# Optimization experiments

Hardware: AMD Instinct MI355X
Metric: run time of the kernel (lower is better)

The kernel has to match this reference:

```python
import jax, jax.numpy as jnp
import numpy as np

N_NODES = 50000
N_EDGES = 800000
STATE_DIM = 128
H1 = 96
H2 = 64


def setup_inputs() -> dict:
    key = jax.random.key(0)
    ks = jax.random.split(key, 10)
    x = jax.random.normal(ks[0], (N_NODES, STATE_DIM), dtype=jnp.float32)
    edge_index = jax.random.randint(ks[1], (2, N_EDGES), 0, N_NODES, dtype=jnp.int64)
    # GCNConv weight [in, out] and bias
    W1 = jax.random.normal(ks[2], (STATE_DIM, H1), dtype=jnp.float32) / np.sqrt(STATE_DIM)
    b1 = jnp.zeros((H1,), dtype=jnp.float32)
    lw1 = jax.random.normal(ks[3], (H1, H1), dtype=jnp.float32) / np.sqrt(H1)
    lb1 = jax.random.normal(ks[4], (H1,), dtype=jnp.float32) * 0.01
    lw2 = jax.random.normal(ks[5], (H1, H2), dtype=jnp.float32) / np.sqrt(H1)
    lb2 = jax.random.normal(ks[6], (H2,), dtype=jnp.float32) * 0.01
    lw3 = jax.random.normal(ks[7], (H2, 1), dtype=jnp.float32) / np.sqrt(H2)
    lb3 = jax.random.normal(ks[8], (1,), dtype=jnp.float32) * 0.01
    return {"x": x, "edge_index": edge_index, "W1": W1, "b1": b1,
            "lw1": lw1, "lb1": lb1, "lw2": lw2, "lb2": lb2, "lw3": lw3, "lb3": lb3}


def reference(x, edge_index, W1, b1, lw1, lb1, lw2, lb2, lw3, lb3):
    N = x.shape[0]
    loop = jnp.arange(N, dtype=edge_index.dtype)
    src = jnp.concatenate([edge_index[0], loop])
    dst = jnp.concatenate([edge_index[1], loop])
    deg = jax.ops.segment_sum(jnp.ones_like(dst, dtype=x.dtype), dst, num_segments=N)
    dinv = jnp.where(deg > 0, jax.lax.rsqrt(jnp.maximum(deg, 1.0)), 0.0)
    norm = dinv[src] * dinv[dst]  # [E+N]
    h = x @ W1  # [N, H1] transform before propagation
    agg = jax.ops.segment_sum(h[src] * norm[:, None], dst, num_segments=N) + b1
    out = jax.nn.relu(agg)            # [N, H1]
    g = jnp.sum(out, axis=0)          # sum pooling over nodes -> [H1]
    g = jax.nn.relu(g @ lw1 + lb1)
    g = jax.nn.relu(g @ lw2 + lb2)
    return g @ lw3 + lb3              # [1]
```

## Files before the change

### kernel.cpp

```cpp
#include <hip/hip_runtime.h>

#define N_NODES 50000
#define N_EDGES 800000
#define D_IN 128
#define H1 96
#define H2 64
#define GEMM_NODES 32
#define SCAN_BLK 256
#define N_SBLK ((N_NODES + SCAN_BLK - 1) / SCAN_BLK)

__global__ void count_deg_kernel(const int* __restrict__ dst, int* __restrict__ deg) {
    int i = blockIdx.x * blockDim.x + threadIdx.x;
    int stride = gridDim.x * blockDim.x;
    for (int e = i; e < N_EDGES; e += stride)
        atomicAdd(&deg[dst[e]], 1);
}

__global__ __launch_bounds__(SCAN_BLK) void deg_part_kernel(const int* __restrict__ deg,
                                                            int* __restrict__ block_sums) {
    __shared__ int s[SCAN_BLK];
    int t = threadIdx.x;
    int i = blockIdx.x * SCAN_BLK + t;
    s[t] = (i < N_NODES) ? deg[i] : 0;
    __syncthreads();
    for (int off = SCAN_BLK / 2; off > 0; off >>= 1) {
        if (t < off) s[t] += s[t + off];
        __syncthreads();
    }
    if (t == 0) block_sums[blockIdx.x] = s[0];
}

__global__ __launch_bounds__(SCAN_BLK) void block_scan_kernel(int* __restrict__ block_sums) {
    __shared__ int s[SCAN_BLK];
    int t = threadIdx.x;
    int v = (t < N_SBLK) ? block_sums[t] : 0;
    s[t] = v;
    __syncthreads();
    for (int off = 1; off < SCAN_BLK; off <<= 1) {
        int u = (t >= off) ? s[t - off] : 0;
        __syncthreads();
        s[t] += u;
        __syncthreads();
    }
    if (t < N_SBLK) block_sums[t] = s[t] - v;
}

__global__ __launch_bounds__(SCAN_BLK) void deg_scan_kernel(const int* __restrict__ deg,
                                                            const int* __restrict__ block_off,
                                                            int* __restrict__ row_start,
                                                            int* __restrict__ cursor,
                                                            float* __restrict__ dinv) {
    __shared__ int s[SCAN_BLK];
    int t = threadIdx.x;
    int i = blockIdx.x * SCAN_BLK + t;
    int v = (i < N_NODES) ? deg[i] : 0;
    s[t] = v;
    __syncthreads();
    for (int off = 1; off < SCAN_BLK; off <<= 1) {
        int u = (t >= off) ? s[t - off] : 0;
        __syncthreads();
        s[t] += u;
        __syncthreads();
    }
    int excl = s[t] - v + block_off[blockIdx.x];
    if (i < N_NODES) {
        row_start[i] = excl;
        cursor[i] = excl;
        dinv[i] = rsqrtf((float)v + 1.0f);
    }
    if (i == 0) row_start[N_NODES] = N_EDGES;
}

__global__ void scatter_kernel(const int* __restrict__ src, const int* __restrict__ dst,
                               int* __restrict__ cursor, int* __restrict__ sorted_src) {
    int i = blockIdx.x * blockDim.x + threadIdx.x;
    int stride = gridDim.x * blockDim.x;
    for (int e = i; e < N_EDGES; e += stride) {
        int d = dst[e];
        int pos = atomicAdd(&cursor[d], 1);
        sorted_src[pos] = src[e];
    }
}

__global__ __launch_bounds__(256) void gemm_kernel(const float* __restrict__ x,
                                                   const float* __restrict__ W1,
                                                   const float* __restrict__ dinv,
                                                   float* __restrict__ hs) {
    __shared__ float sW[D_IN * H1];
    __shared__ float sx[GEMM_NODES * D_IN];
    int tid = threadIdx.x;

    for (int i = tid; i < D_IN * H1 / 4; i += 256)
        ((float4*)sW)[i] = ((const float4*)W1)[i];

    int base = blockIdx.x * GEMM_NODES;
    const float4* x4 = (const float4*)x;
    for (int i = tid; i < GEMM_NODES * D_IN / 4; i += 256) {
        int n = base + i / (D_IN / 4);
        if (n < N_NODES) ((float4*)sx)[i] = x4[(size_t)base * (D_IN / 4) + i];
    }
    __syncthreads();

    int fg = tid & 31;
    int ng = tid >> 5;

    float acc[4][3];
#pragma unroll
    for (int i = 0; i < 4; ++i)
#pragma unroll
        for (int j = 0; j < 3; ++j) acc[i][j] = 0.0f;

#pragma unroll 4
    for (int k = 0; k < D_IN; ++k) {
        float w0 = sW[k * H1 + fg];
        float w1 = sW[k * H1 + fg + 32];
        float w2 = sW[k * H1 + fg + 64];
#pragma unroll
        for (int i = 0; i < 4; ++i) {
            float xv = sx[(ng * 4 + i) * D_IN + k];
            acc[i][0] = fmaf(xv, w0, acc[i][0]);
            acc[i][1] = fmaf(xv, w1, acc[i][1]);
            acc[i][2] = fmaf(xv, w2, acc[i][2]);
        }
    }

#pragma unroll
    for (int i = 0; i < 4; ++i) {
        int n = base + ng * 4 + i;
        if (n < N_NODES) {
            float dv = dinv[n];
            hs[(size_t)n * H1 + fg]      = acc[i][0] * dv;
            hs[(size_t)n * H1 + fg + 32] = acc[i][1] * dv;
            hs[(size_t)n * H1 + fg + 64] = acc[i][2] * dv;
        }
    }
}

__global__ __launch_bounds__(256) void agg_pool_kernel(const float* __restrict__ hs,
                                                       const int* __restrict__ row_start,
                                                       const int* __restrict__ sorted_src,
                                                       const float* __restrict__ dinv,
                                                       const float* __restrict__ b1,
                                                       float* __restrict__ g) {
    int tid = threadIdx.x;
    int grp = tid >> 7;
    int f = tid & 127;
    bool act = f < H1;
    float bf = act ? b1[f] : 0.0f;
    float gacc = 0.0f;

    for (int n = blockIdx.x * 2 + grp; n < N_NODES; n += gridDim.x * 2) {
        float acc = act ? hs[(size_t)n * H1 + f] : 0.0f;
        int e = row_start[n];
        int eend = row_start[n + 1];
        for (; e + 4 <= eend; e += 4) {
            int s0 = sorted_src[e];
            int s1 = sorted_src[e + 1];
            int s2 = sorted_src[e + 2];
            int s3 = sorted_src[e + 3];
            if (act) {
                float v0 = hs[(size_t)s0 * H1 + f];
                float v1 = hs[(size_t)s1 * H1 + f];
                float v2 = hs[(size_t)s2 * H1 + f];
                float v3 = hs[(size_t)s3 * H1 + f];
                acc += (v0 + v1) + (v2 + v3);
            }
        }
        for (; e < eend; ++e) {
            int s = sorted_src[e];
            if (act) acc += hs[(size_t)s * H1 + f];
        }
        if (act) gacc += fmaxf(fmaf(dinv[n], acc, bf), 0.0f);
    }

    __shared__ float sg[H1];
    if (grp == 0 && act) sg[f] = gacc;
    __syncthreads();
    if (grp == 1 && act) atomicAdd(&sg[f], gacc);
    __syncthreads();
    if (grp == 0 && act) atomicAdd(&g[f], sg[f]);
}

__global__ void mlp_kernel(const float* __restrict__ g,
                           const float* __restrict__ lw1, const float* __restrict__ lb1,
                           const float* __restrict__ lw2, const float* __restrict__ lb2,
                           const float* __restrict__ lw3, const float* __restrict__ lb3,
                           float* __restrict__ out) {
    __shared__ float sg[H1], v1[H1], v2[H2];
    int t = threadIdx.x;
    if (t < H1) sg[t] = g[t];
    __syncthreads();
    if (t < H1) {
        float a = lb1[t];
        for (int k = 0; k < H1; ++k) a = fmaf(sg[k], lw1[k * H1 + t], a);
        v1[t] = fmaxf(a, 0.0f);
    }
    __syncthreads();
    if (t < H2) {
        float a = lb2[t];
        for (int k = 0; k < H1; ++k) a = fmaf(v1[k], lw2[k * H2 + t], a);
        v2[t] = fmaxf(a, 0.0f);
    }
    __syncthreads();
    if (t == 0) {
        float a = lb3[0];
        for (int k = 0; k < H2; ++k) a = fmaf(v2[k], lw3[k], a);
        out[0] = a;
    }
}

extern "C" void kernel_launch(void* const* d_in, const int* in_sizes, int n_in,
                              void* d_out, int out_size, void* d_ws, size_t ws_size,
                              hipStream_t stream) {
    const float* x   = (const float*)d_in[0];
    const int*   ei  = (const int*)d_in[1];
    const float* W1  = (const float*)d_in[2];
    const float* b1  = (const float*)d_in[3];
    const float* lw1 = (const float*)d_in[4];
    const float* lb1 = (const float*)d_in[5];
    const float* lw2 = (const float*)d_in[6];
    const float* lb2 = (const float*)d_in[7];
    const float* lw3 = (const float*)d_in[8];
    const float* lb3 = (const float*)d_in[9];
    float* out = (float*)d_out;

    const int* src = ei;
    const int* dst = ei + N_EDGES;

    char* ws = (char*)d_ws;
    size_t off = 0;
    auto alloc = [&](size_t bytes) {
        char* p = ws + off;
        off = (off + bytes + 255) & ~(size_t)255;
        return p;
    };
    int*   deg        = (int*)alloc((size_t)N_NODES * sizeof(int));
    float* g          = (float*)alloc((size_t)H1 * sizeof(float));
    float* dinv       = (float*)alloc((size_t)N_NODES * sizeof(float));
    int*   row_start  = (int*)alloc((size_t)(N_NODES + 1) * sizeof(int));
    int*   cursor     = (int*)alloc((size_t)N_NODES * sizeof(int));
    int*   block_sums = (int*)alloc((size_t)N_SBLK * sizeof(int));
    int*   sorted_src = (int*)alloc((size_t)N_EDGES * sizeof(int));
    float* hs         = (float*)alloc((size_t)N_NODES * H1 * sizeof(float));
    (void)ws_size;

    hipMemsetAsync(deg, 0, (char*)(g + H1) - (char*)deg, stream);

    count_deg_kernel<<<2048, 256, 0, stream>>>(dst, deg);
    deg_part_kernel<<<N_SBLK, SCAN_BLK, 0, stream>>>(deg, block_sums);
    block_scan_kernel<<<1, SCAN_BLK, 0, stream>>>(block_sums);
    deg_scan_kernel<<<N_SBLK, SCAN_BLK, 0, stream>>>(deg, block_sums, row_start, cursor, dinv);
    scatter_kernel<<<2048, 256, 0, stream>>>(src, dst, cursor, sorted_src);

    gemm_kernel<<<(N_NODES + GEMM_NODES - 1) / GEMM_NODES, 256, 0, stream>>>(x, W1, dinv, hs);

    agg_pool_kernel<<<2048, 256, 0, stream>>>(hs, row_start, sorted_src, dinv, b1, g);

    mlp_kernel<<<1, 128, 0, stream>>>(g, lw1, lb1, lw2, lb2, lw3, lb3, out);
}
```

Before: 258.7 us.

## Store transformed node features in bf16 and gather packed pairs per wave

The GEMM output hs is now stored as bf16, which halves the gather traffic of the aggregation kernel. The aggregation is restructured so each 64-lane wave handles one node, with 48 active lanes each reading a packed uint32 holding two features and accumulating in fp32. The intent is to cut memory bandwidth and cache pressure in the random neighbour gather. The cost is reduced precision of the intermediate features and 16 idle lanes per wave.

```diff
diff --git a/kernel.cpp b/kernel.cpp
--- a/kernel.cpp
+++ b/kernel.cpp
@@ -1,13 +1,23 @@
 #include <hip/hip_runtime.h>
+#include <stdint.h>
 
 #define N_NODES 50000
 #define N_EDGES 800000
 #define D_IN 128
 #define H1 96
+#define H1P 48
 #define H2 64
 #define GEMM_NODES 32
 #define SCAN_BLK 256
 #define N_SBLK ((N_NODES + SCAN_BLK - 1) / SCAN_BLK)
+
+__device__ __forceinline__ uint16_t f2bf(float f) {
+    uint32_t u = __float_as_uint(f);
+    uint32_t r = (u + 0x7FFFu + ((u >> 16) & 1u)) >> 16;
+    return (uint16_t)r;
+}
+__device__ __forceinline__ float bf_lo(uint32_t v) { return __uint_as_float(v << 16); }
+__device__ __forceinline__ float bf_hi(uint32_t v) { return __uint_as_float(v & 0xFFFF0000u); }
 
 __global__ void count_deg_kernel(const int* __restrict__ dst, int* __restrict__ deg) {
     int i = blockIdx.x * blockDim.x + threadIdx.x;
@@ -85,7 +95,7 @@
 __global__ __launch_bounds__(256) void gemm_kernel(const float* __restrict__ x,
                                                    const float* __restrict__ W1,
                                                    const float* __restrict__ dinv,
-                                                   float* __restrict__ hs) {
+                                                   uint16_t* __restrict__ hs) {
     __shared__ float sW[D_IN * H1];
     __shared__ float sx[GEMM_NODES * D_IN];
     int tid = threadIdx.x;
@@ -129,56 +139,77 @@
         int n = base + ng * 4 + i;
         if (n < N_NODES) {
             float dv = dinv[n];
-            hs[(size_t)n * H1 + fg]      = acc[i][0] * dv;
-            hs[(size_t)n * H1 + fg + 32] = acc[i][1] * dv;
-            hs[(size_t)n * H1 + fg + 64] = acc[i][2] * dv;
-        }
-    }
-}
-
-__global__ __launch_bounds__(256) void agg_pool_kernel(const float* __restrict__ hs,
+            hs[(size_t)n * H1 + fg]      = f2bf(acc[i][0] * dv);
+            hs[(size_t)n * H1 + fg + 32] = f2bf(acc[i][1] * dv);
+            hs[(size_t)n * H1 + fg + 64] = f2bf(acc[i][2] * dv);
+        }
+    }
+}
+
+__global__ __launch_bounds__(256) void agg_pool_kernel(const uint32_t* __restrict__ hs2,
                                                        const int* __restrict__ row_start,
                                                        const int* __restrict__ sorted_src,
                                                        const float* __restrict__ dinv,
                                                        const float* __restrict__ b1,
                                                        float* __restrict__ g) {
     int tid = threadIdx.x;
-    int grp = tid >> 7;
-    int f = tid & 127;
-    bool act = f < H1;
-    float bf = act ? b1[f] : 0.0f;
-    float gacc = 0.0f;
-
-    for (int n = blockIdx.x * 2 + grp; n < N_NODES; n += gridDim.x * 2) {
-        float acc = act ? hs[(size_t)n * H1 + f] : 0.0f;
+    int wave = tid >> 6;
+    int j = tid & 63;
+    bool act = j < H1P;
+    float b0 = 0.0f, b1v = 0.0f;
+    if (act) { b0 = b1[2 * j]; b1v = b1[2 * j + 1]; }
+    float g0 = 0.0f, g1 = 0.0f;
+
+    int wid = blockIdx.x * 4 + wave;
+    int nw = gridDim.x * 4;
+    for (int n = wid; n < N_NODES; n += nw) {
+        float a0 = 0.0f, a1 = 0.0f;
+        if (act) {
+            uint32_t v = hs2[n * H1P + j];
+            a0 = bf_lo(v); a1 = bf_hi(v);
+        }
         int e = row_start[n];
-        int eend = row_start[n + 1];
-        for (; e + 4 <= eend; e += 4) {
+        int ee = row_start[n + 1];
+        for (; e + 4 <= ee; e += 4) {
             int s0 = sorted_src[e];
             int s1 = sorted_src[e + 1];
             int s2 = sorted_src[e + 2];
             int s3 = sorted_src[e + 3];
             if (act) {
-                float v0 = hs[(size_t)s0 * H1 + f];
-                float v1 = hs[(size_t)s1 * H1 + f];
-                float v2 = hs[(size_t)s2 * H1 + f];
-                float v3 = hs[(size_t)s3 * H1 + f];
-                acc += (v0 + v1) + (v2 + v3);
+                uint32_t v0 = hs2[s0 * H1P + j];
+                uint32_t v1 = hs2[s1 * H1P + j];
+                uint32_t v2 = hs2[s2 * H1P + j];
+                uint32_t v3 = hs2[s3 * H1P + j];
+                a0 += (bf_lo(v0) + bf_lo(v1)) + (bf_lo(v2) + bf_lo(v3));
+                a1 += (bf_hi(v0) + bf_hi(v1)) + (bf_hi(v2) + bf_hi(v3));
             }
         }
-        for (; e < eend; ++e) {
+        for (; e < ee; ++e) {
             int s = sorted_src[e];
-            if (act) acc += hs[(size_t)s * H1 + f];
-        }
-        if (act) gacc += fmaxf(fmaf(dinv[n], acc, bf), 0.0f);
+            if (act) {
+                uint32_t v = hs2[s * H1P + j];
+                a0 += bf_lo(v); a1 += bf_hi(v);
+            }
+        }
+        float dv = dinv[n];
+        if (act) {
+            g0 += fmaxf(fmaf(dv, a0, b0), 0.0f);
+            g1 += fmaxf(fmaf(dv, a1, b1v), 0.0f);
+        }
     }
 
     __shared__ float sg[H1];
-    if (grp == 0 && act) sg[f] = gacc;
-    __syncthreads();
-    if (grp == 1 && act) atomicAdd(&sg[f], gacc);
-    __syncthreads();
-    if (grp == 0 && act) atomicAdd(&g[f], sg[f]);
+    if (wave == 0 && act) { sg[2 * j] = g0; sg[2 * j + 1] = g1; }
+    __syncthreads();
+    if (wave != 0 && act) {
+        atomicAdd(&sg[2 * j], g0);
+        atomicAdd(&sg[2 * j + 1], g1);
+    }
+    __syncthreads();
+    if (wave == 0 && act) {
+        atomicAdd(&g[2 * j], sg[2 * j]);
+        atomicAdd(&g[2 * j + 1], sg[2 * j + 1]);
+    }
 }
 
 __global__ void mlp_kernel(const float* __restrict__ g,
@@ -234,14 +265,14 @@
         off = (off + bytes + 255) & ~(size_t)255;
         return p;
     };
-    int*   deg        = (int*)alloc((size_t)N_NODES * sizeof(int));
-    float* g          = (float*)alloc((size_t)H1 * sizeof(float));
-    float* dinv       = (float*)alloc((size_t)N_NODES * sizeof(float));
-    int*   row_start  = (int*)alloc((size_t)(N_NODES + 1) * sizeof(int));
-    int*   cursor     = (int*)alloc((size_t)N_NODES * sizeof(int));
-    int*   block_sums = (int*)alloc((size_t)N_SBLK * sizeof(int));
-    int*   sorted_src = (int*)alloc((size_t)N_EDGES * sizeof(int));
-    float* hs         = (float*)alloc((size_t)N_NODES * H1 * sizeof(float));
+    int*      deg        = (int*)alloc((size_t)N_NODES * sizeof(int));
+    float*    g          = (float*)alloc((size_t)H1 * sizeof(float));
+    float*    dinv       = (float*)alloc((size_t)N_NODES * sizeof(float));
+    int*      row_start  = (int*)alloc((size_t)(N_NODES + 1) * sizeof(int));
+    int*      cursor     = (int*)alloc((size_t)N_NODES * sizeof(int));
+    int*      block_sums = (int*)alloc((size_t)N_SBLK * sizeof(int));
+    int*      sorted_src = (int*)alloc((size_t)N_EDGES * sizeof(int));
+    uint16_t* hs         = (uint16_t*)alloc((size_t)N_NODES * H1 * sizeof(uint16_t));
     (void)ws_size;
 
     hipMemsetAsync(deg, 0, (char*)(g + H1) - (char*)deg, stream);
@@ -254,7 +285,7 @@
 
     gemm_kernel<<<(N_NODES + GEMM_NODES - 1) / GEMM_NODES, 256, 0, stream>>>(x, W1, dinv, hs);
 
-    agg_pool_kernel<<<2048, 256, 0, stream>>>(hs, row_start, sorted_src, dinv, b1, g);
+    agg_pool_kernel<<<2048, 256, 0, stream>>>((const uint32_t*)hs, row_start, sorted_src, dinv, b1, g);
 
     mlp_kernel<<<1, 128, 0, stream>>>(g, lw1, lb1, lw2, lb2, lw3, lb3, out);
 }
```

After: 278.2 us. 1.08x slower.

## Fuse GEMM with degree count and scatter with dinv scaling via block partitioning

Applied to the files above, without the earlier changes.

The GEMM is merged with degree counting into one launch that assigns block ranges by role. The dinv row scaling moves out of the GEMM into a second role-split kernel alongside the CSR scatter, so the GEMM no longer waits on the degree scan. The goal is fewer launches and concurrency between compute-bound and atomic-bound work. In exchange, h is re-read and re-written for scaling, an extra 19 MB of traffic. The MLP also stages its weights in shared memory.

```diff
diff --git a/kernel.cpp b/kernel.cpp
--- a/kernel.cpp
+++ b/kernel.cpp
@@ -1,4 +1,5 @@
 #include <hip/hip_runtime.h>
+#include <stdint.h>
 
 #define N_NODES 50000
 #define N_EDGES 800000
@@ -6,14 +7,79 @@
 #define H1 96
 #define H2 64
 #define GEMM_NODES 32
+#define GEMM_BLOCKS ((N_NODES + GEMM_NODES - 1) / GEMM_NODES)
+#define COUNT_BLOCKS 256
 #define SCAN_BLK 256
 #define N_SBLK ((N_NODES + SCAN_BLK - 1) / SCAN_BLK)
-
-__global__ void count_deg_kernel(const int* __restrict__ dst, int* __restrict__ deg) {
-    int i = blockIdx.x * blockDim.x + threadIdx.x;
-    int stride = gridDim.x * blockDim.x;
-    for (int e = i; e < N_EDGES; e += stride)
-        atomicAdd(&deg[dst[e]], 1);
+#define SCAT_BLOCKS 2048
+#define SCALE_BLOCKS 512
+
+__global__ __launch_bounds__(256) void k1_gemm_count(const float* __restrict__ x,
+                                                     const float* __restrict__ W1,
+                                                     float* __restrict__ h,
+                                                     const int* __restrict__ dst,
+                                                     int* __restrict__ deg) {
+    __shared__ float sW[D_IN * H1];
+    __shared__ float sx[GEMM_NODES * D_IN];
+    int tid = threadIdx.x;
+
+    if (blockIdx.x < GEMM_BLOCKS) {
+        for (int i = tid; i < D_IN * H1 / 4; i += 256)
+            ((float4*)sW)[i] = ((const float4*)W1)[i];
+
+        int base = blockIdx.x * GEMM_NODES;
+        const float4* x4 = (const float4*)x;
+        for (int i = tid; i < GEMM_NODES * D_IN / 4; i += 256) {
+            int n = base + i / (D_IN / 4);
+            if (n < N_NODES) ((float4*)sx)[i] = x4[(size_t)base * (D_IN / 4) + i];
+        }
+        __syncthreads();
+
+        int fg = tid & 31;
+        int ng = tid >> 5;
+
+        float acc[4][3];
+#pragma unroll
+        for (int i = 0; i < 4; ++i)
+#pragma unroll
+            for (int j = 0; j < 3; ++j) acc[i][j] = 0.0f;
+
+#pragma unroll 4
+        for (int k = 0; k < D_IN; ++k) {
+            float w0 = sW[k * H1 + fg];
+            float w1 = sW[k * H1 + fg + 32];
+            float w2 = sW[k * H1 + fg + 64];
+#pragma unroll
+            for (int i = 0; i < 4; ++i) {
+                float xv = sx[(ng * 4 + i) * D_IN + k];
+                acc[i][0] = fmaf(xv, w0, acc[i][0]);
+                acc[i][1] = fmaf(xv, w1, acc[i][1]);
+                acc[i][2] = fmaf(xv, w2, acc[i][2]);
+            }
+        }
+
+#pragma unroll
+        for (int i = 0; i < 4; ++i) {
+            int n = base + ng * 4 + i;
+            if (n < N_NODES) {
+                h[(size_t)n * H1 + fg]      = acc[i][0];
+                h[(size_t)n * H1 + fg + 32] = acc[i][1];
+                h[(size_t)n * H1 + fg + 64] = acc[i][2];
+            }
+        }
+    } else {
+        int bid = blockIdx.x - GEMM_BLOCKS;
+        int gid = bid * 256 + tid;
+        int stride = COUNT_BLOCKS * 256;
+        const int4* d4 = (const int4*)dst;
+        for (int i = gid; i < N_EDGES / 4; i += stride) {
+            int4 d = d4[i];
+            atomicAdd(&deg[d.x], 1);
+            atomicAdd(&deg[d.y], 1);
+            atomicAdd(&deg[d.z], 1);
+            atomicAdd(&deg[d.w], 1);
+        }
+    }
 }
 
 __global__ __launch_bounds__(SCAN_BLK) void deg_part_kernel(const int* __restrict__ deg,
@@ -71,67 +137,33 @@
     if (i == 0) row_start[N_NODES] = N_EDGES;
 }
 
-__global__ void scatter_kernel(const int* __restrict__ src, const int* __restrict__ dst,
-                               int* __restrict__ cursor, int* __restrict__ sorted_src) {
-    int i = blockIdx.x * blockDim.x + threadIdx.x;
-    int stride = gridDim.x * blockDim.x;
-    for (int e = i; e < N_EDGES; e += stride) {
-        int d = dst[e];
-        int pos = atomicAdd(&cursor[d], 1);
-        sorted_src[pos] = src[e];
-    }
-}
-
-__global__ __launch_bounds__(256) void gemm_kernel(const float* __restrict__ x,
-                                                   const float* __restrict__ W1,
-                                                   const float* __restrict__ dinv,
-                                                   float* __restrict__ hs) {
-    __shared__ float sW[D_IN * H1];
-    __shared__ float sx[GEMM_NODES * D_IN];
+__global__ __launch_bounds__(256) void k3_scatter_scale(const int* __restrict__ src,
+                                                        const int* __restrict__ dst,
+                                                        int* __restrict__ cursor,
+                                                        int* __restrict__ sorted_src,
+                                                        float* __restrict__ h,
+                                                        const float* __restrict__ dinv) {
     int tid = threadIdx.x;
-
-    for (int i = tid; i < D_IN * H1 / 4; i += 256)
-        ((float4*)sW)[i] = ((const float4*)W1)[i];
-
-    int base = blockIdx.x * GEMM_NODES;
-    const float4* x4 = (const float4*)x;
-    for (int i = tid; i < GEMM_NODES * D_IN / 4; i += 256) {
-        int n = base + i / (D_IN / 4);
-        if (n < N_NODES) ((float4*)sx)[i] = x4[(size_t)base * (D_IN / 4) + i];
-    }
-    __syncthreads();
-
-    int fg = tid & 31;
-    int ng = tid >> 5;
-
-    float acc[4][3];
-#pragma unroll
-    for (int i = 0; i < 4; ++i)
-#pragma unroll
-        for (int j = 0; j < 3; ++j) acc[i][j] = 0.0f;
-
-#pragma unroll 4
-    for (int k = 0; k < D_IN; ++k) {
-        float w0 = sW[k * H1 + fg];
-        float w1 = sW[k * H1 + fg + 32];
-        float w2 = sW[k * H1 + fg + 64];
-#pragma unroll
-        for (int i = 0; i < 4; ++i) {
-            float xv = sx[(ng * 4 + i) * D_IN + k];
-            acc[i][0] = fmaf(xv, w0, acc[i][0]);
-            acc[i][1] = fmaf(xv, w1, acc[i][1]);
-            acc[i][2] = fmaf(xv, w2, acc[i][2]);
-        }
-    }
-
-#pragma unroll
-    for (int i = 0; i < 4; ++i) {
-        int n = base + ng * 4 + i;
-        if (n < N_NODES) {
+    if (blockIdx.x < SCAT_BLOCKS) {
+        int gid = blockIdx.x * 256 + tid;
+        int stride = SCAT_BLOCKS * 256;
+        for (int e = gid; e < N_EDGES; e += stride) {
+            int d = dst[e];
+            int pos = atomicAdd(&cursor[d], 1);
+            sorted_src[pos] = src[e];
+        }
+    } else {
+        int bid = blockIdx.x - SCAT_BLOCKS;
+        int gid = bid * 256 + tid;
+        int stride = SCALE_BLOCKS * 256;
+        float4* h4 = (float4*)h;
+        const int TOT = N_NODES * (H1 / 4);
+        for (int i = gid; i < TOT; i += stride) {
+            int n = i / (H1 / 4);
             float dv = dinv[n];
-            hs[(size_t)n * H1 + fg]      = acc[i][0] * dv;
-            hs[(size_t)n * H1 + fg + 32] = acc[i][1] * dv;
-            hs[(size_t)n * H1 + fg + 64] = acc[i][2] * dv;
+            float4 v = h4[i];
+            v.x *= dv; v.y *= dv; v.z *= dv; v.w *= dv;
+            h4[i] = v;
         }
     }
 }
@@ -181,30 +213,41 @@
     if (grp == 0 && act) atomicAdd(&g[f], sg[f]);
 }
 
-__global__ void mlp_kernel(const float* __restrict__ g,
+__global__ __launch_bounds__(256) void mlp_kernel(const float* __restrict__ g,
                            const float* __restrict__ lw1, const float* __restrict__ lb1,
                            const float* __restrict__ lw2, const float* __restrict__ lb2,
                            const float* __restrict__ lw3, const float* __restrict__ lb3,
                            float* __restrict__ out) {
+    __shared__ float slw1[H1 * H1];
+    __shared__ float slw2[H1 * H2];
+    __shared__ float slw3[H2];
     __shared__ float sg[H1], v1[H1], v2[H2];
     int t = threadIdx.x;
+    for (int i = t; i < H1 * H1 / 4; i += 256)
+        ((float4*)slw1)[i] = ((const float4*)lw1)[i];
+    for (int i = t; i < H1 * H2 / 4; i += 256)
+        ((float4*)slw2)[i] = ((const float4*)lw2)[i];
+    if (t < H2) slw3[t] = lw3[t];
     if (t < H1) sg[t] = g[t];
     __syncthreads();
     if (t < H1) {
         float a = lb1[t];
-        for (int k = 0; k < H1; ++k) a = fmaf(sg[k], lw1[k * H1 + t], a);
+#pragma unroll 8
+        for (int k = 0; k < H1; ++k) a = fmaf(sg[k], slw1[k * H1 + t], a);
         v1[t] = fmaxf(a, 0.0f);
     }
     __syncthreads();
     if (t < H2) {
         float a = lb2[t];
-        for (int k = 0; k < H1; ++k) a = fmaf(v1[k], lw2[k * H2 + t], a);
+#pragma unroll 8
+        for (int k = 0; k < H1; ++k) a = fmaf(v1[k], slw2[k * H2 + t], a);
         v2[t] = fmaxf(a, 0.0f);
     }
     __syncthreads();
     if (t == 0) {
         float a = lb3[0];
-        for (int k = 0; k < H2; ++k) a = fmaf(v2[k], lw3[k], a);
+#pragma unroll 8
+        for (int k = 0; k < H2; ++k) a = fmaf(v2[k], slw3[k], a);
         out[0] = a;
     }
 }
@@ -241,20 +284,20 @@
     int*   cursor     = (int*)alloc((size_t)N_NODES * sizeof(int));
     int*   block_sums = (int*)alloc((size_t)N_SBLK * sizeof(int));
     int*   sorted_src = (int*)alloc((size_t)N_EDGES * sizeof(int));
-    float* hs         = (float*)alloc((size_t)N_NODES * H1 * sizeof(float));
+    float* h          = (float*)alloc((size_t)N_NODES * H1 * sizeof(float));
     (void)ws_size;
 
     hipMemsetAsync(deg, 0, (char*)(g + H1) - (char*)deg, stream);
 
-    count_deg_kernel<<<2048, 256, 0, stream>>>(dst, deg);
+    k1_gemm_count<<<GEMM_BLOCKS + COUNT_BLOCKS, 256, 0, stream>>>(x, W1, h, dst, deg);
+
     deg_part_kernel<<<N_SBLK, SCAN_BLK, 0, stream>>>(deg, block_sums);
     block_scan_kernel<<<1, SCAN_BLK, 0, stream>>>(block_sums);
     deg_scan_kernel<<<N_SBLK, SCAN_BLK, 0, stream>>>(deg, block_sums, row_start, cursor, dinv);
-    scatter_kernel<<<2048, 256, 0, stream>>>(src, dst, cursor, sorted_src);
-
-    gemm_kernel<<<(N_NODES + GEMM_NODES - 1) / GEMM_NODES, 256, 0, stream>>>(x, W1, dinv, hs);
-
-    agg_pool_kernel<<<2048, 256, 0, stream>>>(hs, row_start, sorted_src, dinv, b1, g);
-
-    mlp_kernel<<<1, 128, 0, stream>>>(g, lw1, lb1, lw2, lb2, lw3, lb3, out);
-}
+
+    k3_scatter_scale<<<SCAT_BLOCKS + SCALE_BLOCKS, 256, 0, stream>>>(src, dst, cursor, sorted_src, h, dinv);
+
+    agg_pool_kernel<<<2048, 256, 0, stream>>>(h, row_start, sorted_src, dinv, b1, g);
+
+    mlp_kernel<<<1, 256, 0, stream>>>(g, lw1, lb1, lw2, lb2, lw3, lb3, out);
+}
```

Result: faster. 248.3 us (-4.0%).

## Fuse scatter with GEMM, fold MLP into last aggregation block, vectorize degree count

Applied to the files above, without the earlier changes.

The edge scatter and the x@W1 GEMM now run as disjoint block ranges of one horizontally fused launch, so they can overlap. The GEMM reads W1 from global memory instead of staging it in LDS, which cuts LDS use per block and allows higher occupancy, at the cost of more global/L1 traffic. The MLP kernel is removed: the last block of the aggregation kernel, found through an atomic done counter, runs it. The degree count reads dst as int4 with fewer blocks.

```diff
diff --git a/kernel.cpp b/kernel.cpp
--- a/kernel.cpp
+++ b/kernel.cpp
@@ -1,4 +1,5 @@
 #include <hip/hip_runtime.h>
+#include <stdint.h>
 
 #define N_NODES 50000
 #define N_EDGES 800000
@@ -6,14 +7,24 @@
 #define H1 96
 #define H2 64
 #define GEMM_NODES 32
+#define GEMM_BLOCKS ((N_NODES + GEMM_NODES - 1) / GEMM_NODES)
+#define COUNT_BLOCKS 1024
 #define SCAN_BLK 256
 #define N_SBLK ((N_NODES + SCAN_BLK - 1) / SCAN_BLK)
+#define SCAT_BLOCKS 2048
+#define AGG_BLOCKS 2048
 
 __global__ void count_deg_kernel(const int* __restrict__ dst, int* __restrict__ deg) {
-    int i = blockIdx.x * blockDim.x + threadIdx.x;
-    int stride = gridDim.x * blockDim.x;
-    for (int e = i; e < N_EDGES; e += stride)
-        atomicAdd(&deg[dst[e]], 1);
+    int gid = blockIdx.x * 256 + threadIdx.x;
+    int stride = COUNT_BLOCKS * 256;
+    const int4* d4 = (const int4*)dst;
+    for (int i = gid; i < N_EDGES / 4; i += stride) {
+        int4 d = d4[i];
+        atomicAdd(&deg[d.x], 1);
+        atomicAdd(&deg[d.y], 1);
+        atomicAdd(&deg[d.z], 1);
+        atomicAdd(&deg[d.w], 1);
+    }
 }
 
 __global__ __launch_bounds__(SCAN_BLK) void deg_part_kernel(const int* __restrict__ deg,
@@ -71,67 +82,67 @@
     if (i == 0) row_start[N_NODES] = N_EDGES;
 }
 
-__global__ void scatter_kernel(const int* __restrict__ src, const int* __restrict__ dst,
-                               int* __restrict__ cursor, int* __restrict__ sorted_src) {
-    int i = blockIdx.x * blockDim.x + threadIdx.x;
-    int stride = gridDim.x * blockDim.x;
-    for (int e = i; e < N_EDGES; e += stride) {
-        int d = dst[e];
-        int pos = atomicAdd(&cursor[d], 1);
-        sorted_src[pos] = src[e];
-    }
-}
-
-__global__ __launch_bounds__(256) void gemm_kernel(const float* __restrict__ x,
-                                                   const float* __restrict__ W1,
-                                                   const float* __restrict__ dinv,
-                                                   float* __restrict__ hs) {
-    __shared__ float sW[D_IN * H1];
+__global__ __launch_bounds__(256) void k2_scatter_gemm(const int* __restrict__ src,
+                                                       const int* __restrict__ dst,
+                                                       int* __restrict__ cursor,
+                                                       int* __restrict__ sorted_src,
+                                                       const float* __restrict__ x,
+                                                       const float* __restrict__ W1,
+                                                       const float* __restrict__ dinv,
+                                                       float* __restrict__ hs) {
     __shared__ float sx[GEMM_NODES * D_IN];
     int tid = threadIdx.x;
 
-    for (int i = tid; i < D_IN * H1 / 4; i += 256)
-        ((float4*)sW)[i] = ((const float4*)W1)[i];
-
-    int base = blockIdx.x * GEMM_NODES;
-    const float4* x4 = (const float4*)x;
-    for (int i = tid; i < GEMM_NODES * D_IN / 4; i += 256) {
-        int n = base + i / (D_IN / 4);
-        if (n < N_NODES) ((float4*)sx)[i] = x4[(size_t)base * (D_IN / 4) + i];
-    }
-    __syncthreads();
-
-    int fg = tid & 31;
-    int ng = tid >> 5;
-
-    float acc[4][3];
-#pragma unroll
-    for (int i = 0; i < 4; ++i)
-#pragma unroll
-        for (int j = 0; j < 3; ++j) acc[i][j] = 0.0f;
+    if (blockIdx.x < SCAT_BLOCKS) {
+        int gid = blockIdx.x * 256 + tid;
+        int stride = SCAT_BLOCKS * 256;
+        for (int e = gid; e < N_EDGES; e += stride) {
+            int d = dst[e];
+            int pos = atomicAdd(&cursor[d], 1);
+            sorted_src[pos] = src[e];
+        }
+    } else {
+        int gblk = blockIdx.x - SCAT_BLOCKS;
+        int base = gblk * GEMM_NODES;
+        const float4* x4 = (const float4*)x;
+        for (int i = tid; i < GEMM_NODES * D_IN / 4; i += 256) {
+            int n = base + i / (D_IN / 4);
+            if (n < N_NODES) ((float4*)sx)[i] = x4[(size_t)base * (D_IN / 4) + i];
+        }
+        __syncthreads();
+
+        int fg = tid & 31;
+        int ng = tid >> 5;
+
+        float acc[4][3];
+#pragma unroll
+        for (int i = 0; i < 4; ++i)
+#pragma unroll
+            for (int j = 0; j < 3; ++j) acc[i][j] = 0.0f;
 
 #pragma unroll 4
-    for (int k = 0; k < D_IN; ++k) {
-        float w0 = sW[k * H1 + fg];
-        float w1 = sW[k * H1 + fg + 32];
-        float w2 = sW[k * H1 + fg + 64];
+        for (int k = 0; k < D_IN; ++k) {
+            float w0 = W1[k * H1 + fg];
+            float w1 = W1[k * H1 + fg + 32];
+            float w2 = W1[k * H1 + fg + 64];
+#pragma unroll
+            for (int i = 0; i < 4; ++i) {
+                float xv = sx[(ng * 4 + i) * D_IN + k];
+                acc[i][0] = fmaf(xv, w0, acc[i][0]);
+                acc[i][1] = fmaf(xv, w1, acc[i][1]);
+                acc[i][2] = fmaf(xv, w2, acc[i][2]);
+            }
+        }
+
 #pragma unroll
         for (int i = 0; i < 4; ++i) {
-            float xv = sx[(ng * 4 + i) * D_IN + k];
-            acc[i][0] = fmaf(xv, w0, acc[i][0]);
-            acc[i][1] = fmaf(xv, w1, acc[i][1]);
-            acc[i][2] = fmaf(xv, w2, acc[i][2]);
-        }
-    }
-
-#pragma unroll
-    for (int i = 0; i < 4; ++i) {
-        int n = base + ng * 4 + i;
-        if (n < N_NODES) {
-            float dv = dinv[n];
-            hs[(size_t)n * H1 + fg]      = acc[i][0] * dv;
-            hs[(size_t)n * H1 + fg + 32] = acc[i][1] * dv;
-            hs[(size_t)n * H1 + fg + 64] = acc[i][2] * dv;
+            int n = base + ng * 4 + i;
+            if (n < N_NODES) {
+                float dv = dinv[n];
+                hs[(size_t)n * H1 + fg]      = acc[i][0] * dv;
+                hs[(size_t)n * H1 + fg + 32] = acc[i][1] * dv;
+                hs[(size_t)n * H1 + fg + 64] = acc[i][2] * dv;
+            }
         }
     }
 }
@@ -141,7 +152,12 @@
                                                        const int* __restrict__ sorted_src,
                                                        const float* __restrict__ dinv,
                                                        const float* __restrict__ b1,
-                                                       float* __restrict__ g) {
+                                                       float* __restrict__ g,
+                                                       int* __restrict__ done,
+                                                       const float* __restrict__ lw1, const float* __restrict__ lb1,
+                                                       const float* __restrict__ lw2, const float* __restrict__ lb2,
+                                                       const float* __restrict__ lw3, const float* __restrict__ lb3,
+                                                       float* __restrict__ out) {
     int tid = threadIdx.x;
     int grp = tid >> 7;
     int f = tid & 127;
@@ -179,33 +195,39 @@
     if (grp == 1 && act) atomicAdd(&sg[f], gacc);
     __syncthreads();
     if (grp == 0 && act) atomicAdd(&g[f], sg[f]);
-}
-
-__global__ void mlp_kernel(const float* __restrict__ g,
-                           const float* __restrict__ lw1, const float* __restrict__ lb1,
-                           const float* __restrict__ lw2, const float* __restrict__ lb2,
-                           const float* __restrict__ lw3, const float* __restrict__ lb3,
-                           float* __restrict__ out) {
-    __shared__ float sg[H1], v1[H1], v2[H2];
-    int t = threadIdx.x;
-    if (t < H1) sg[t] = g[t];
-    __syncthreads();
-    if (t < H1) {
-        float a = lb1[t];
-        for (int k = 0; k < H1; ++k) a = fmaf(sg[k], lw1[k * H1 + t], a);
-        v1[t] = fmaxf(a, 0.0f);
-    }
-    __syncthreads();
-    if (t < H2) {
-        float a = lb2[t];
-        for (int k = 0; k < H1; ++k) a = fmaf(v1[k], lw2[k * H2 + t], a);
-        v2[t] = fmaxf(a, 0.0f);
-    }
-    __syncthreads();
-    if (t == 0) {
-        float a = lb3[0];
-        for (int k = 0; k < H2; ++k) a = fmaf(v2[k], lw3[k], a);
-        out[0] = a;
+
+    __shared__ int is_last;
+    if (tid == 0) {
+        __threadfence();
+        int old = atomicAdd(done, 1);
+        is_last = (old == (int)gridDim.x - 1) ? 1 : 0;
+        if (is_last) __threadfence();
+    }
+    __syncthreads();
+    if (!is_last) return;
+
+    __shared__ float fg_[H1], v1[H1], v2[H2];
+    if (tid < H1) fg_[tid] = g[tid];
+    __syncthreads();
+    if (tid < H1) {
+        float a = lb1[tid];
+#pragma unroll 8
+        for (int k = 0; k < H1; ++k) a = fmaf(fg_[k], lw1[k * H1 + tid], a);
+        v1[tid] = fmaxf(a, 0.0f);
+    }
+    __syncthreads();
+    if (tid < H2) {
+        float a = lb2[tid];
+#pragma unroll 8
+        for (int k = 0; k < H1; ++k) a = fmaf(v1[k], lw2[k * H2 + tid], a);
+        v2[tid] = fmaxf(a, 0.0f);
+    }
+    __syncthreads();
+    if (tid < 64) {
+        float pr = v2[tid] * lw3[tid];
+#pragma unroll
+        for (int off = 32; off > 0; off >>= 1) pr += __shfl_down(pr, off, 64);
+        if (tid == 0) out[0] = pr + lb3[0];
     }
 }
 
@@ -236,6 +258,7 @@
     };
     int*   deg        = (int*)alloc((size_t)N_NODES * sizeof(int));
     float* g          = (float*)alloc((size_t)H1 * sizeof(float));
+    int*   done       = (int*)alloc(sizeof(int));
     float* dinv       = (float*)alloc((size_t)N_NODES * sizeof(float));
     int*   row_start  = (int*)alloc((size_t)(N_NODES + 1) * sizeof(int));
     int*   cursor     = (int*)alloc((size_t)N_NODES * sizeof(int));
@@ -244,17 +267,16 @@
     float* hs         = (float*)alloc((size_t)N_NODES * H1 * sizeof(float));
     (void)ws_size;
 
-    hipMemsetAsync(deg, 0, (char*)(g + H1) - (char*)deg, stream);
-
-    count_deg_kernel<<<2048, 256, 0, stream>>>(dst, deg);
+    hipMemsetAsync(deg, 0, (char*)(done + 1) - (char*)deg, stream);
+
+    count_deg_kernel<<<COUNT_BLOCKS, 256, 0, stream>>>(dst, deg);
     deg_part_kernel<<<N_SBLK, SCAN_BLK, 0, stream>>>(deg, block_sums);
     block_scan_kernel<<<1, SCAN_BLK, 0, stream>>>(block_sums);
     deg_scan_kernel<<<N_SBLK, SCAN_BLK, 0, stream>>>(deg, block_sums, row_start, cursor, dinv);
-    scatter_kernel<<<2048, 256, 0, stream>>>(src, dst, cursor, sorted_src);
-
-    gemm_kernel<<<(N_NODES + GEMM_NODES - 1) / GEMM_NODES, 256, 0, stream>>>(x, W1, dinv, hs);
-
-    agg_pool_kernel<<<2048, 256, 0, stream>>>(hs, row_start, sorted_src, dinv, b1, g);
-
-    mlp_kernel<<<1, 128, 0, stream>>>(g, lw1, lb1, lw2, lb2, lw3, lb3, out);
-}
+
+    k2_scatter_gemm<<<SCAT_BLOCKS + GEMM_BLOCKS, 256, 0, stream>>>(src, dst, cursor, sorted_src,
+                                                                   x, W1, dinv, hs);
+
+    agg_pool_kernel<<<AGG_BLOCKS, 256, 0, stream>>>(hs, row_start, sorted_src, dinv, b1, g, done,
+                                                    lw1, lb1, lw2, lb2, lw3, lb3, out);
+}
```

New measurement: 251.1 us. 2.9% less time.
